# Kernel optimization log

Measured on AMD Instinct MI355X. Metric: run time of the kernel, lower is better.

The kernel has to match this reference:

```python
import jax, jax.numpy as jnp
import numpy as np

D_MODEL = 1024
HEADS = 16
HEAD_DIM = D_MODEL // HEADS


def setup_inputs() -> dict:
    key = jax.random.key(0)
    k_x, k_q, k_k, k_v, k_o = jax.random.split(key, 5)
    B, S = 4, 2048
    return {
        "x": jax.random.normal(k_x, (B, S, D_MODEL), dtype=jnp.float32),
        "W_q": jax.random.normal(k_q, (D_MODEL, D_MODEL), dtype=jnp.float32),
        "W_k": jax.random.normal(k_k, (D_MODEL, D_MODEL), dtype=jnp.float32),
        "W_v": jax.random.normal(k_v, (D_MODEL, D_MODEL), dtype=jnp.float32),
        "fc_out": jax.random.normal(k_o, (D_MODEL, D_MODEL), dtype=jnp.float32),
    }


def reference(x, W_q, W_k, W_v, fc_out):
    B, S, D = x.shape
    H, Hd = HEADS, HEAD_DIM
    # QKV projections (no bias)
    Q = jnp.matmul(x, W_q)  # [B,S,D]
    K = jnp.matmul(x, W_k)
    V = jnp.matmul(x, W_v)
    # split heads -> [B,H,S,Hd]
    Qh = Q.reshape(B, S, H, Hd).transpose(0, 2, 1, 3)
    Kh = K.reshape(B, S, H, Hd).transpose(0, 2, 1, 3)
    Vh = V.reshape(B, S, H, Hd).transpose(0, 2, 1, 3)
    # full unfused attention: materialize [B,H,S,S] scores, softmax over last dim
    scores = jnp.einsum("bhqd,bhkd->bhqk", Qh, Kh) / jnp.sqrt(jnp.float32(Hd))
    attn = jax.nn.softmax(scores, axis=-1)
    head_out = jnp.einsum("bhqk,bhkd->bhqd", attn, Vh)  # [B,H,S,Hd]
    merged = head_out.transpose(0, 2, 1, 3).reshape(B, S, D)
    return jnp.matmul(merged, fc_out)
```

## Files before the change

kernel.cpp:

```cpp
#include <hip/hip_runtime.h>
#include <stdint.h>

#define MROWS 8192
#define DM    1024
#define NH    16
#define HD    64
#define SEQ   2048

typedef __bf16 bf16x8 __attribute__((ext_vector_type(8)));
typedef __bf16 bf16x4 __attribute__((ext_vector_type(4)));
typedef float  floatx4 __attribute__((ext_vector_type(4)));

#define QSCALE 0.18033688011112042f

__device__ __forceinline__ int xcd_swz512(int bid) {
  return ((bid & 7) << 6) | (bid >> 3);
}

__device__ __forceinline__ void async16(const void* g, void* l) {
  __builtin_amdgcn_global_load_lds(
      (__attribute__((address_space(1))) void*)g,
      (__attribute__((address_space(3))) void*)l,
      16, 0, 0);
}

__device__ __forceinline__ floatx4 mfma16(bf16x8 a, bf16x8 b, floatx4 c) {
  return __builtin_amdgcn_mfma_f32_16x16x32_bf16(a, b, c, 0, 0, 0);
}


__global__ void __launch_bounds__(256) split_x_kernel(const float* __restrict__ x,
                                                      __bf16* __restrict__ xh,
                                                      __bf16* __restrict__ xl) {
  const int i = blockIdx.x * 256 + threadIdx.x;
  const float4 v = reinterpret_cast<const float4*>(x)[i];
  const float vv[4] = {v.x, v.y, v.z, v.w};
  bf16x4 H, L;
#pragma unroll
  for (int j = 0; j < 4; ++j) {
    const __bf16 h = (__bf16)vv[j];
    H[j] = h;
    L[j] = (__bf16)(vv[j] - (float)h);
  }
  reinterpret_cast<bf16x4*>(xh)[i] = H;
  reinterpret_cast<bf16x4*>(xl)[i] = L;
}

__global__ void __launch_bounds__(256) wtrans4_kernel(
    const float* __restrict__ Wq, const float* __restrict__ Wk,
    const float* __restrict__ Wv, const float* __restrict__ Wf,
    __bf16* __restrict__ Tqh, __bf16* __restrict__ Tql,
    __bf16* __restrict__ Tkh, __bf16* __restrict__ Tkl,
    __bf16* __restrict__ Tvh, __bf16* __restrict__ Tfh) {
  const int which = blockIdx.x >> 10;
  const int blk = blockIdx.x & 1023;
  const float* W = (which == 0) ? Wq : (which == 1) ? Wk : (which == 2) ? Wv : Wf;
  __bf16* Th = (which == 0) ? Tqh : (which == 1) ? Tkh : (which == 2) ? Tvh : Tfh;
  __bf16* Tl = (which == 0) ? Tql : (which == 1) ? Tkl : (__bf16*)nullptr;

  __shared__ float t[32][33];
  const int tx = threadIdx.x & 31, ty = threadIdx.x >> 5;
  const int bx = blk & 31, by = blk >> 5;
#pragma unroll
  for (int j = 0; j < 4; ++j) {
    const int k = by * 32 + ty + j * 8;
    t[ty + j * 8][tx] = W[(size_t)k * DM + bx * 32 + tx];
  }
  __syncthreads();
#pragma unroll
  for (int j = 0; j < 4; ++j) {
    const int n = bx * 32 + ty + j * 8;
    const int k = by * 32 + tx;
    const float v = t[tx][ty + j * 8];
    const __bf16 h = (__bf16)v;
    Th[(size_t)n * DM + k] = h;
    if (Tl) Tl[(size_t)n * DM + k] = (__bf16)(v - (float)h);
  }
}

template <int OUTMODE>
__global__ void __launch_bounds__(256) gemm_nt(const __bf16* __restrict__ Ah,
                                               const __bf16* __restrict__ Bh,
                                               void* __restrict__ C0) {
  __shared__ __align__(16) __bf16 sAh[128 * 32];
  __shared__ __align__(16) __bf16 sBh[128 * 32];

  const int tid = threadIdx.x;
  const int lid = xcd_swz512(blockIdx.x);
  const int bm = lid >> 3;
  const int bn = lid & 7;
  const int m0 = bm << 7, n0 = bn << 7;
  const int w = tid >> 6;
  const int lane = tid & 63;
  const int wm = (w >> 1) << 6;
  const int wn = (w & 1) << 6;
  const int lm = lane & 15;
  const int q4 = lane >> 4;

  floatx4 acc[4][4];
  const floatx4 fz = {0.f, 0.f, 0.f, 0.f};
#pragma unroll
  for (int i = 0; i < 4; ++i)
#pragma unroll
    for (int j = 0; j < 4; ++j) acc[i][j] = fz;

  const int c0 = tid, c1 = tid + 256;
  const int row0 = c0 >> 2, cc0 = (c0 & 3) ^ ((row0 >> 1) & 3);
  const int row1 = c1 >> 2, cc1 = (c1 & 3) ^ ((row1 >> 1) & 3);

  int offA[4], offB[4];
#pragma unroll
  for (int i = 0; i < 4; ++i) {
    const int ra = wm + i * 16 + lm;
    offA[i] = ra * 32 + ((q4 ^ ((ra >> 1) & 3)) << 3);
    const int rb = wn + i * 16 + lm;
    offB[i] = rb * 32 + ((q4 ^ ((rb >> 1) & 3)) << 3);
  }

  size_t ga0 = (size_t)(m0 + row0) * DM + cc0 * 8;
  size_t gb0 = (size_t)(n0 + row0) * DM + cc0 * 8;
  size_t ga1 = (size_t)(m0 + row1) * DM + cc1 * 8;
  size_t gb1 = (size_t)(n0 + row1) * DM + cc1 * 8;

  for (int it = 0; it < 32; ++it) {
    async16(Ah + ga0, &sAh[c0 * 8]);
    async16(Bh + gb0, &sBh[c0 * 8]);
    async16(Ah + ga1, &sAh[c1 * 8]);
    async16(Bh + gb1, &sBh[c1 * 8]);
    ga0 += 32; gb0 += 32; ga1 += 32; gb1 += 32;
    __syncthreads();

    bf16x8 ah[4], bh[4];
#pragma unroll
    for (int i = 0; i < 4; ++i) {
      ah[i] = *(const bf16x8*)&sAh[offA[i]];
      bh[i] = *(const bf16x8*)&sBh[offB[i]];
    }
#pragma unroll
    for (int i = 0; i < 4; ++i)
#pragma unroll
      for (int j = 0; j < 4; ++j)
        acc[i][j] = mfma16(ah[i], bh[j], acc[i][j]);
    __syncthreads();
  }

#pragma unroll
  for (int i = 0; i < 4; ++i) {
#pragma unroll
    for (int j = 0; j < 4; ++j) {
#pragma unroll
      for (int r = 0; r < 4; ++r) {
        const int gr = m0 + wm + i * 16 + q4 * 4 + r;
        const int gc = n0 + wn + j * 16 + lm;
        const float v = acc[i][j][r];
        if constexpr (OUTMODE == 1) {
          ((float*)C0)[(size_t)gr * DM + gc] = v;
        } else {
          const int bb = gr >> 11, ss = gr & 2047;
          const int s6 = ss & 63;
          const int sp = (ss & ~63) | (s6 & 32) | ((s6 & 12) << 1) |
                         ((s6 & 16) >> 2) | (s6 & 3);
          const int hh = gc >> 6, dd = gc & 63;
          ((__bf16*)C0)[(((size_t)(bb * NH + hh) << 6) + dd) * SEQ + sp] = (__bf16)v;
        }
      }
    }
  }
}

__global__ void __launch_bounds__(256, 2) gemm_qk(const __bf16* __restrict__ Ah,
                                                  const __bf16* __restrict__ Al,
                                                  const __bf16* __restrict__ Bqh,
                                                  const __bf16* __restrict__ Bql,
                                                  const __bf16* __restrict__ Bkh,
                                                  const __bf16* __restrict__ Bkl,
                                                  __bf16* __restrict__ Qh,
                                                  __bf16* __restrict__ Ql,
                                                  __bf16* __restrict__ Kh,
                                                  __bf16* __restrict__ Kl) {
  __shared__ __align__(16) __bf16 sAh[128 * 32];
  __shared__ __align__(16) __bf16 sAl[128 * 32];
  __shared__ __align__(16) __bf16 sQh_[128 * 32];
  __shared__ __align__(16) __bf16 sQl_[128 * 32];
  __shared__ __align__(16) __bf16 sKh_[128 * 32];
  __shared__ __align__(16) __bf16 sKl_[128 * 32];

  const int tid = threadIdx.x;
  const int lid = xcd_swz512(blockIdx.x);
  const int bm = lid >> 3;
  const int bn = lid & 7;
  const int m0 = bm << 7, n0 = bn << 7;
  const int w = tid >> 6;
  const int lane = tid & 63;
  const int wm = (w >> 1) << 6;
  const int wn = (w & 1) << 6;
  const int lm = lane & 15;
  const int q4 = lane >> 4;

  floatx4 accq[4][4], acck[4][4];
  const floatx4 fz = {0.f, 0.f, 0.f, 0.f};
#pragma unroll
  for (int i = 0; i < 4; ++i)
#pragma unroll
    for (int j = 0; j < 4; ++j) { accq[i][j] = fz; acck[i][j] = fz; }

  const int c0 = tid, c1 = tid + 256;
  const int row0 = c0 >> 2, cc0 = (c0 & 3) ^ ((row0 >> 1) & 3);
  const int row1 = c1 >> 2, cc1 = (c1 & 3) ^ ((row1 >> 1) & 3);

  int offA[4], offB[4];
#pragma unroll
  for (int i = 0; i < 4; ++i) {
    const int ra = wm + i * 16 + lm;
    offA[i] = ra * 32 + ((q4 ^ ((ra >> 1) & 3)) << 3);
    const int rb = wn + i * 16 + lm;
    offB[i] = rb * 32 + ((q4 ^ ((rb >> 1) & 3)) << 3);
  }

  size_t ga0 = (size_t)(m0 + row0) * DM + cc0 * 8;
  size_t gb0 = (size_t)(n0 + row0) * DM + cc0 * 8;
  size_t ga1 = (size_t)(m0 + row1) * DM + cc1 * 8;
  size_t gb1 = (size_t)(n0 + row1) * DM + cc1 * 8;

  for (int it = 0; it < 32; ++it) {
    async16(Ah + ga0, &sAh[c0 * 8]);
    async16(Al + ga0, &sAl[c0 * 8]);
    async16(Ah + ga1, &sAh[c1 * 8]);
    async16(Al + ga1, &sAl[c1 * 8]);
    async16(Bqh + gb0, &sQh_[c0 * 8]);
    async16(Bql + gb0, &sQl_[c0 * 8]);
    async16(Bqh + gb1, &sQh_[c1 * 8]);
    async16(Bql + gb1, &sQl_[c1 * 8]);
    async16(Bkh + gb0, &sKh_[c0 * 8]);
    async16(Bkl + gb0, &sKl_[c0 * 8]);
    async16(Bkh + gb1, &sKh_[c1 * 8]);
    async16(Bkl + gb1, &sKl_[c1 * 8]);
    ga0 += 32; gb0 += 32; ga1 += 32; gb1 += 32;
    __syncthreads();

    bf16x8 ah[4], al[4];
#pragma unroll
    for (int i = 0; i < 4; ++i) {
      ah[i] = *(const bf16x8*)&sAh[offA[i]];
      al[i] = *(const bf16x8*)&sAl[offA[i]];
    }
    {
      bf16x8 bh[4], bl[4];
#pragma unroll
      for (int j = 0; j < 4; ++j) {
        bh[j] = *(const bf16x8*)&sQh_[offB[j]];
        bl[j] = *(const bf16x8*)&sQl_[offB[j]];
      }
#pragma unroll
      for (int i = 0; i < 4; ++i)
#pragma unroll
        for (int j = 0; j < 4; ++j) {
          accq[i][j] = mfma16(ah[i], bh[j], accq[i][j]);
          accq[i][j] = mfma16(ah[i], bl[j], accq[i][j]);
          accq[i][j] = mfma16(al[i], bh[j], accq[i][j]);
        }
    }
    {
      bf16x8 bh[4], bl[4];
#pragma unroll
      for (int j = 0; j < 4; ++j) {
        bh[j] = *(const bf16x8*)&sKh_[offB[j]];
        bl[j] = *(const bf16x8*)&sKl_[offB[j]];
      }
#pragma unroll
      for (int i = 0; i < 4; ++i)
#pragma unroll
        for (int j = 0; j < 4; ++j) {
          acck[i][j] = mfma16(ah[i], bh[j], acck[i][j]);
          acck[i][j] = mfma16(ah[i], bl[j], acck[i][j]);
          acck[i][j] = mfma16(al[i], bh[j], acck[i][j]);
        }
    }
    __syncthreads();
  }

#pragma unroll
  for (int i = 0; i < 4; ++i) {
#pragma unroll
    for (int j = 0; j < 4; ++j) {
#pragma unroll
      for (int r = 0; r < 4; ++r) {
        const int gr = m0 + wm + i * 16 + q4 * 4 + r;
        const int gc = n0 + wn + j * 16 + lm;
        const size_t idx = (size_t)gr * DM + gc;
        const float vq = accq[i][j][r] * QSCALE;
        const __bf16 qhv = (__bf16)vq;
        Qh[idx] = qhv;
        Ql[idx] = (__bf16)(vq - (float)qhv);
        const float vk = acck[i][j][r];
        const __bf16 khv = (__bf16)vk;
        Kh[idx] = khv;
        Kl[idx] = (__bf16)(vk - (float)khv);
      }
    }
  }
}

__global__ void __launch_bounds__(256, 2) flash_kernel(const __bf16* __restrict__ Qh,
                                                       const __bf16* __restrict__ Ql,
                                                       const __bf16* __restrict__ Kh,
                                                       const __bf16* __restrict__ Kl,
                                                       const __bf16* __restrict__ Vt,
                                                       __bf16* __restrict__ Mg) {
  __shared__ __align__(16) __bf16 sKh[2][64 * 64];
  __shared__ __align__(16) __bf16 sKl[2][64 * 64];
  __shared__ __align__(16) __bf16 sV[2][64 * 64];

  const int tid = threadIdx.x;
  const int lid = xcd_swz512(blockIdx.x);
  const int qt = lid & 7;
  const int bh = lid >> 3;
  const int b = bh >> 4;
  const int h = bh & 15;
  const int mq0 = b * SEQ + qt * 256;
  const int ch = h * 64;
  const int w = tid >> 6;
  const int lane = tid & 63;
  const int lm = lane & 15;
  const int q4 = lane >> 4;

  const int c0 = tid, c1 = tid + 256;
  const int r0 = c0 >> 3, e0 = ((c0 & 7) ^ (r0 & 7)) << 3;
  const int r1 = c1 >> 3, e1 = ((c1 & 7) ^ (r1 & 7)) << 3;

  size_t gk0 = (size_t)(b * SEQ + r0) * DM + ch + e0;
  size_t gk1 = (size_t)(b * SEQ + r1) * DM + ch + e1;
  size_t gv0 = (size_t)(bh * 64 + r0) * SEQ + e0;
  size_t gv1 = (size_t)(bh * 64 + r1) * SEQ + e1;

  async16(Kh + gk0, &sKh[0][c0 * 8]);
  async16(Kl + gk0, &sKl[0][c0 * 8]);
  async16(Kh + gk1, &sKh[0][c1 * 8]);
  async16(Kl + gk1, &sKl[0][c1 * 8]);
  async16(Vt + gv0, &sV[0][c0 * 8]);
  async16(Vt + gv1, &sV[0][c1 * 8]);
  gk0 += (size_t)64 * DM;
  gk1 += (size_t)64 * DM;
  gv0 += 64;
  gv1 += 64;

  bf16x8 qh[4][2], ql[4][2];
#pragma unroll
  for (int mi = 0; mi < 4; ++mi) {
    const size_t qrow = (size_t)(mq0 + w * 64 + mi * 16 + lm) * DM + ch;
#pragma unroll
    for (int ks = 0; ks < 2; ++ks) {
      qh[mi][ks] = *(const bf16x8*)&Qh[qrow + ks * 32 + q4 * 8];
      ql[mi][ks] = *(const bf16x8*)&Ql[qrow + ks * 32 + q4 * 8];
    }
  }

  int ofr[2][4];
#pragma unroll
  for (int ks = 0; ks < 2; ++ks)
#pragma unroll
    for (int t = 0; t < 4; ++t) {
      const int rk = t * 16 + lm;
      ofr[ks][t] = rk * 64 + (((ks * 4 + q4) ^ (rk & 7)) << 3);
    }

  floatx4 o[4][4];
  const floatx4 fz = {0.f, 0.f, 0.f, 0.f};
#pragma unroll
  for (int mi = 0; mi < 4; ++mi)
#pragma unroll
    for (int dt = 0; dt < 4; ++dt) o[mi][dt] = fz;
  float lsum[4] = {0.f, 0.f, 0.f, 0.f};
  float m[4] = {-1e30f, -1e30f, -1e30f, -1e30f};

  for (int it = 0; it < 32; ++it) {
    const int cur = it & 1;
    asm volatile("s_waitcnt vmcnt(0)" ::: "memory");
    __builtin_amdgcn_s_barrier();
    __builtin_amdgcn_sched_barrier(0);
    if (it < 31) {
      const int nxt = cur ^ 1;
      async16(Kh + gk0, &sKh[nxt][c0 * 8]);
      async16(Kl + gk0, &sKl[nxt][c0 * 8]);
      async16(Kh + gk1, &sKh[nxt][c1 * 8]);
      async16(Kl + gk1, &sKl[nxt][c1 * 8]);
      async16(Vt + gv0, &sV[nxt][c0 * 8]);
      async16(Vt + gv1, &sV[nxt][c1 * 8]);
      gk0 += (size_t)64 * DM;
      gk1 += (size_t)64 * DM;
      gv0 += 64;
      gv1 += 64;
    }
    const __bf16* bKh = sKh[cur];
    const __bf16* bKl = sKl[cur];
    const __bf16* bV = sV[cur];

    floatx4 s2[4][4];
#pragma unroll
    for (int nt = 0; nt < 4; ++nt)
#pragma unroll
      for (int mi = 0; mi < 4; ++mi) s2[nt][mi] = fz;
#pragma unroll
    for (int ks = 0; ks < 2; ++ks) {
#pragma unroll
      for (int nt = 0; nt < 4; ++nt) {
        const bf16x8 kh = *(const bf16x8*)&bKh[ofr[ks][nt]];
        const bf16x8 kl = *(const bf16x8*)&bKl[ofr[ks][nt]];
#pragma unroll
        for (int mi = 0; mi < 4; ++mi) {
          s2[nt][mi] = mfma16(kh, qh[mi][ks], s2[nt][mi]);
          s2[nt][mi] = mfma16(kl, qh[mi][ks], s2[nt][mi]);
          s2[nt][mi] = mfma16(kh, ql[mi][ks], s2[nt][mi]);
        }
      }
    }

    float tm[4];
    bool need = false;
#pragma unroll
    for (int mi = 0; mi < 4; ++mi) {
      float mx = fmaxf(fmaxf(s2[0][mi][0], s2[0][mi][1]),
                       fmaxf(s2[0][mi][2], s2[0][mi][3]));
#pragma unroll
      for (int nt = 1; nt < 4; ++nt) {
        mx = fmaxf(mx, fmaxf(fmaxf(s2[nt][mi][0], s2[nt][mi][1]),
                             fmaxf(s2[nt][mi][2], s2[nt][mi][3])));
      }
      mx = fmaxf(mx, __shfl_xor(mx, 16));
      mx = fmaxf(mx, __shfl_xor(mx, 32));
      tm[mi] = mx;
      need = need || (mx > m[mi] + 8.f);
    }
    if (__ballot(need)) {
#pragma unroll
      for (int mi = 0; mi < 4; ++mi) {
        const float mn = fmaxf(m[mi], tm[mi]);
        const float a = __builtin_amdgcn_exp2f(m[mi] - mn);
        m[mi] = mn;
        lsum[mi] *= a;
#pragma unroll
        for (int dt = 0; dt < 4; ++dt) o[mi][dt] *= a;
      }
    }

    bf16x8 aP[4][2];
#pragma unroll
    for (int mi = 0; mi < 4; ++mi) {
      float ps = 0.f;
#pragma unroll
      for (int nt = 0; nt < 4; ++nt) {
#pragma unroll
        for (int r = 0; r < 4; ++r) {
          const float p = __builtin_amdgcn_exp2f(s2[nt][mi][r] - m[mi]);
          ps += p;
          aP[mi][nt >> 1][(nt & 1) * 4 + r] = (__bf16)p;
        }
      }
      ps += __shfl_xor(ps, 16);
      ps += __shfl_xor(ps, 32);
      lsum[mi] += ps;
    }

#pragma unroll
    for (int ks = 0; ks < 2; ++ks) {
#pragma unroll
      for (int dt = 0; dt < 4; ++dt) {
        const bf16x8 bv = *(const bf16x8*)&bV[ofr[ks][dt]];
#pragma unroll
        for (int mi = 0; mi < 4; ++mi)
          o[mi][dt] = mfma16(bv, aP[mi][ks], o[mi][dt]);
      }
    }
  }

#pragma unroll
  for (int mi = 0; mi < 4; ++mi) {
    const float inv = __builtin_amdgcn_rcpf(lsum[mi]);
    const int gr = mq0 + w * 64 + mi * 16 + lm;
#pragma unroll
    for (int dt = 0; dt < 4; ++dt) {
      bf16x4 ov;
#pragma unroll
      for (int r = 0; r < 4; ++r) ov[r] = (__bf16)(o[mi][dt][r] * inv);
      *(bf16x4*)&Mg[(size_t)gr * DM + ch + dt * 16 + q4 * 4] = ov;
    }
  }
}


extern "C" void kernel_launch(void* const* d_in, const int* in_sizes, int n_in,
                              void* d_out, int out_size, void* d_ws, size_t ws_size,
                              hipStream_t stream) {
  (void)in_sizes; (void)n_in; (void)out_size; (void)ws_size;
  const float* x  = (const float*)d_in[0];
  const float* Wq = (const float*)d_in[1];
  const float* Wk = (const float*)d_in[2];
  const float* Wv = (const float*)d_in[3];
  const float* fc = (const float*)d_in[4];
  float* out = (float*)d_out;

  char* base = (char*)d_ws;
  const size_t XB = (size_t)MROWS * DM * 2;
  const size_t WB = (size_t)DM * DM * 2;
  __bf16* xh  = (__bf16*)(base);
  __bf16* xl  = (__bf16*)(base + XB);
  __bf16* wqh = (__bf16*)(base + 2 * XB);
  __bf16* wql = (__bf16*)(base + 2 * XB + WB);
  __bf16* wkh = (__bf16*)(base + 2 * XB + 2 * WB);
  __bf16* wkl = (__bf16*)(base + 2 * XB + 3 * WB);
  __bf16* wvh = (__bf16*)(base + 2 * XB + 4 * WB);
  __bf16* fch = (__bf16*)(base + 2 * XB + 5 * WB);
  __bf16* Qh  = (__bf16*)(base + 2 * XB + 6 * WB);
  __bf16* Ql  = (__bf16*)(base + 3 * XB + 6 * WB);
  __bf16* Kh  = (__bf16*)(base + 4 * XB + 6 * WB);
  __bf16* Kl  = (__bf16*)(base + 5 * XB + 6 * WB);
  __bf16* Vt  = xl;
  __bf16* Mg  = xh;

  split_x_kernel<<<dim3(8192), dim3(256), 0, stream>>>(x, xh, xl);
  wtrans4_kernel<<<dim3(4096), dim3(256), 0, stream>>>(Wq, Wk, Wv, fc,
                                                       wqh, wql, wkh, wkl, wvh, fch);

  gemm_qk<<<dim3(512), dim3(256), 0, stream>>>(xh, xl, wqh, wql, wkh, wkl, Qh, Ql, Kh, Kl);
  gemm_nt<3><<<dim3(512), dim3(256), 0, stream>>>(xh, wvh, (void*)Vt);

  flash_kernel<<<dim3(512), dim3(256), 0, stream>>>(Qh, Ql, Kh, Kl, Vt, Mg);

  gemm_nt<1><<<dim3(512), dim3(256), 0, stream>>>(Mg, fch, (void*)out);
}
```

Before: 372.1 us.

## Fuse V projection into Q/K GEMM kernel sharing the x tile loads

Result: slower. 384.4 us (+3.3%).

```diff
diff --git a/kernel.cpp b/kernel.cpp
--- a/kernel.cpp
+++ b/kernel.cpp
@@ -244,37 +244,27 @@
       ah[i] = *(const bf16x8*)&sAh[offA[i]];
       al[i] = *(const bf16x8*)&sAl[offA[i]];
     }
-    {
-      bf16x8 bh[4], bl[4];
-#pragma unroll
-      for (int j = 0; j < 4; ++j) {
-        bh[j] = *(const bf16x8*)&sQh_[offB[j]];
-        bl[j] = *(const bf16x8*)&sQl_[offB[j]];
-      }
-#pragma unroll
-      for (int i = 0; i < 4; ++i)
-#pragma unroll
-        for (int j = 0; j < 4; ++j) {
-          accq[i][j] = mfma16(ah[i], bh[j], accq[i][j]);
-          accq[i][j] = mfma16(ah[i], bl[j], accq[i][j]);
-          accq[i][j] = mfma16(al[i], bh[j], accq[i][j]);
-        }
-    }
-    {
-      bf16x8 bh[4], bl[4];
-#pragma unroll
-      for (int j = 0; j < 4; ++j) {
-        bh[j] = *(const bf16x8*)&sKh_[offB[j]];
-        bl[j] = *(const bf16x8*)&sKl_[offB[j]];
-      }
-#pragma unroll
-      for (int i = 0; i < 4; ++i)
-#pragma unroll
-        for (int j = 0; j < 4; ++j) {
-          acck[i][j] = mfma16(ah[i], bh[j], acck[i][j]);
-          acck[i][j] = mfma16(ah[i], bl[j], acck[i][j]);
-          acck[i][j] = mfma16(al[i], bh[j], acck[i][j]);
-        }
+#pragma unroll
+    for (int j = 0; j < 4; ++j) {
+      const bf16x8 bh = *(const bf16x8*)&sQh_[offB[j]];
+      const bf16x8 bl = *(const bf16x8*)&sQl_[offB[j]];
+#pragma unroll
+      for (int i = 0; i < 4; ++i) {
+        accq[i][j] = mfma16(ah[i], bh, accq[i][j]);
+        accq[i][j] = mfma16(ah[i], bl, accq[i][j]);
+        accq[i][j] = mfma16(al[i], bh, accq[i][j]);
+      }
+    }
+#pragma unroll
+    for (int j = 0; j < 4; ++j) {
+      const bf16x8 bh = *(const bf16x8*)&sKh_[offB[j]];
+      const bf16x8 bl = *(const bf16x8*)&sKl_[offB[j]];
+#pragma unroll
+      for (int i = 0; i < 4; ++i) {
+        acck[i][j] = mfma16(ah[i], bh, acck[i][j]);
+        acck[i][j] = mfma16(ah[i], bl, acck[i][j]);
+        acck[i][j] = mfma16(al[i], bh, acck[i][j]);
+      }
     }
     __syncthreads();
   }
@@ -296,6 +286,147 @@
         const __bf16 khv = (__bf16)vk;
         Kh[idx] = khv;
         Kl[idx] = (__bf16)(vk - (float)khv);
+      }
+    }
+  }
+}
+
+__global__ void __launch_bounds__(256, 2) gemm_qkv(const __bf16* __restrict__ Ah,
+                                                   const __bf16* __restrict__ Al,
+                                                   const __bf16* __restrict__ Bqh,
+                                                   const __bf16* __restrict__ Bql,
+                                                   const __bf16* __restrict__ Bkh,
+                                                   const __bf16* __restrict__ Bkl,
+                                                   const __bf16* __restrict__ Bvh,
+                                                   __bf16* __restrict__ Qh,
+                                                   __bf16* __restrict__ Ql,
+                                                   __bf16* __restrict__ Kh,
+                                                   __bf16* __restrict__ Kl,
+                                                   __bf16* __restrict__ Vt) {
+  __shared__ __align__(16) __bf16 sAh[128 * 32];
+  __shared__ __align__(16) __bf16 sAl[128 * 32];
+  __shared__ __align__(16) __bf16 sQh_[128 * 32];
+  __shared__ __align__(16) __bf16 sQl_[128 * 32];
+  __shared__ __align__(16) __bf16 sKh_[128 * 32];
+  __shared__ __align__(16) __bf16 sKl_[128 * 32];
+  __shared__ __align__(16) __bf16 sVh_[128 * 32];
+
+  const int tid = threadIdx.x;
+  const int lid = xcd_swz512(blockIdx.x);
+  const int bm = lid >> 3;
+  const int bn = lid & 7;
+  const int m0 = bm << 7, n0 = bn << 7;
+  const int w = tid >> 6;
+  const int lane = tid & 63;
+  const int wm = (w >> 1) << 6;
+  const int wn = (w & 1) << 6;
+  const int lm = lane & 15;
+  const int q4 = lane >> 4;
+
+  floatx4 accq[4][4], acck[4][4], accv[4][4];
+  const floatx4 fz = {0.f, 0.f, 0.f, 0.f};
+#pragma unroll
+  for (int i = 0; i < 4; ++i)
+#pragma unroll
+    for (int j = 0; j < 4; ++j) { accq[i][j] = fz; acck[i][j] = fz; accv[i][j] = fz; }
+
+  const int c0 = tid, c1 = tid + 256;
+  const int row0 = c0 >> 2, cc0 = (c0 & 3) ^ ((row0 >> 1) & 3);
+  const int row1 = c1 >> 2, cc1 = (c1 & 3) ^ ((row1 >> 1) & 3);
+
+  int offA[4], offB[4];
+#pragma unroll
+  for (int i = 0; i < 4; ++i) {
+    const int ra = wm + i * 16 + lm;
+    offA[i] = ra * 32 + ((q4 ^ ((ra >> 1) & 3)) << 3);
+    const int rb = wn + i * 16 + lm;
+    offB[i] = rb * 32 + ((q4 ^ ((rb >> 1) & 3)) << 3);
+  }
+
+  size_t ga0 = (size_t)(m0 + row0) * DM + cc0 * 8;
+  size_t gb0 = (size_t)(n0 + row0) * DM + cc0 * 8;
+  size_t ga1 = (size_t)(m0 + row1) * DM + cc1 * 8;
+  size_t gb1 = (size_t)(n0 + row1) * DM + cc1 * 8;
+
+  for (int it = 0; it < 32; ++it) {
+    async16(Ah + ga0, &sAh[c0 * 8]);
+    async16(Al + ga0, &sAl[c0 * 8]);
+    async16(Ah + ga1, &sAh[c1 * 8]);
+    async16(Al + ga1, &sAl[c1 * 8]);
+    async16(Bqh + gb0, &sQh_[c0 * 8]);
+    async16(Bql + gb0, &sQl_[c0 * 8]);
+    async16(Bqh + gb1, &sQh_[c1 * 8]);
+    async16(Bql + gb1, &sQl_[c1 * 8]);
+    async16(Bkh + gb0, &sKh_[c0 * 8]);
+    async16(Bkl + gb0, &sKl_[c0 * 8]);
+    async16(Bkh + gb1, &sKh_[c1 * 8]);
+    async16(Bkl + gb1, &sKl_[c1 * 8]);
+    async16(Bvh + gb0, &sVh_[c0 * 8]);
+    async16(Bvh + gb1, &sVh_[c1 * 8]);
+    ga0 += 32; gb0 += 32; ga1 += 32; gb1 += 32;
+    __syncthreads();
+
+    bf16x8 ah[4], al[4];
+#pragma unroll
+    for (int i = 0; i < 4; ++i) {
+      ah[i] = *(const bf16x8*)&sAh[offA[i]];
+      al[i] = *(const bf16x8*)&sAl[offA[i]];
+    }
+#pragma unroll
+    for (int j = 0; j < 4; ++j) {
+      const bf16x8 bv = *(const bf16x8*)&sVh_[offB[j]];
+#pragma unroll
+      for (int i = 0; i < 4; ++i)
+        accv[i][j] = mfma16(ah[i], bv, accv[i][j]);
+    }
+#pragma unroll
+    for (int j = 0; j < 4; ++j) {
+      const bf16x8 bh = *(const bf16x8*)&sQh_[offB[j]];
+      const bf16x8 bl = *(const bf16x8*)&sQl_[offB[j]];
+#pragma unroll
+      for (int i = 0; i < 4; ++i) {
+        accq[i][j] = mfma16(ah[i], bh, accq[i][j]);
+        accq[i][j] = mfma16(ah[i], bl, accq[i][j]);
+        accq[i][j] = mfma16(al[i], bh, accq[i][j]);
+      }
+    }
+#pragma unroll
+    for (int j = 0; j < 4; ++j) {
+      const bf16x8 bh = *(const bf16x8*)&sKh_[offB[j]];
+      const bf16x8 bl = *(const bf16x8*)&sKl_[offB[j]];
+#pragma unroll
+      for (int i = 0; i < 4; ++i) {
+        acck[i][j] = mfma16(ah[i], bh, acck[i][j]);
+        acck[i][j] = mfma16(ah[i], bl, acck[i][j]);
+        acck[i][j] = mfma16(al[i], bh, acck[i][j]);
+      }
+    }
+    __syncthreads();
+  }
+
+#pragma unroll
+  for (int i = 0; i < 4; ++i) {
+#pragma unroll
+    for (int j = 0; j < 4; ++j) {
+#pragma unroll
+      for (int r = 0; r < 4; ++r) {
+        const int gr = m0 + wm + i * 16 + q4 * 4 + r;
+        const int gc = n0 + wn + j * 16 + lm;
+        const size_t idx = (size_t)gr * DM + gc;
+        const float vq = accq[i][j][r] * QSCALE;
+        const __bf16 qhv = (__bf16)vq;
+        Qh[idx] = qhv;
+        Ql[idx] = (__bf16)(vq - (float)qhv);
+        const float vk = acck[i][j][r];
+        const __bf16 khv = (__bf16)vk;
+        Kh[idx] = khv;
+        Kl[idx] = (__bf16)(vk - (float)khv);
+        const int bb = gr >> 11, ss = gr & 2047;
+        const int s6 = ss & 63;
+        const int sp = (ss & ~63) | (s6 & 32) | ((s6 & 12) << 1) |
+                       ((s6 & 16) >> 2) | (s6 & 3);
+        const int hh = gc >> 6, dd = gc & 63;
+        Vt[(((size_t)(bb * NH + hh) << 6) + dd) * SEQ + sp] = (__bf16)accv[i][j][r];
       }
     }
   }
@@ -491,7 +622,7 @@
 extern "C" void kernel_launch(void* const* d_in, const int* in_sizes, int n_in,
                               void* d_out, int out_size, void* d_ws, size_t ws_size,
                               hipStream_t stream) {
-  (void)in_sizes; (void)n_in; (void)out_size; (void)ws_size;
+  (void)in_sizes; (void)n_in; (void)out_size;
   const float* x  = (const float*)d_in[0];
   const float* Wq = (const float*)d_in[1];
   const float* Wk = (const float*)d_in[2];
@@ -514,15 +645,24 @@
   __bf16* Ql  = (__bf16*)(base + 3 * XB + 6 * WB);
   __bf16* Kh  = (__bf16*)(base + 4 * XB + 6 * WB);
   __bf16* Kl  = (__bf16*)(base + 5 * XB + 6 * WB);
-  __bf16* Vt  = xl;
   __bf16* Mg  = xh;
 
   split_x_kernel<<<dim3(8192), dim3(256), 0, stream>>>(x, xh, xl);
   wtrans4_kernel<<<dim3(4096), dim3(256), 0, stream>>>(Wq, Wk, Wv, fc,
                                                        wqh, wql, wkh, wkl, wvh, fch);
 
-  gemm_qk<<<dim3(512), dim3(256), 0, stream>>>(xh, xl, wqh, wql, wkh, wkl, Qh, Ql, Kh, Kl);
-  gemm_nt<3><<<dim3(512), dim3(256), 0, stream>>>(xh, wvh, (void*)Vt);
+  const size_t need = 7 * XB + 6 * WB;
+  __bf16* Vt;
+  if (ws_size >= need) {
+    Vt = (__bf16*)(base + 6 * XB + 6 * WB);
+    gemm_qkv<<<dim3(512), dim3(256), 0, stream>>>(xh, xl, wqh, wql, wkh, wkl, wvh,
+                                                  Qh, Ql, Kh, Kl, Vt);
+  } else {
+    Vt = xl;
+    gemm_qk<<<dim3(512), dim3(256), 0, stream>>>(xh, xl, wqh, wql, wkh, wkl,
+                                                 Qh, Ql, Kh, Kl);
+    gemm_nt<3><<<dim3(512), dim3(256), 0, stream>>>(xh, wvh, (void*)Vt);
+  }
 
   flash_kernel<<<dim3(512), dim3(256), 0, stream>>>(Qh, Ql, Kh, Kl, Vt, Mg);
 
```
